# Performance work log

Measured on AMD Instinct MI355X. Metric: run time of the kernel, lower is better.

## Reference

```python
import jax, jax.numpy as jnp
import numpy as np

DIM = 1024
HEAD_DIM = 64
NUM_HEADS = DIM // HEAD_DIM
SCALE = HEAD_DIM ** -0.5
B, N, M = 2, 1024, 2048


def setup_inputs() -> dict:
    key = jax.random.key(0)
    ks = jax.random.split(key, 7)
    x = jax.random.normal(ks[0], (B, N, DIM), dtype=jnp.float32)
    context = jax.random.normal(ks[1], (B, M, DIM), dtype=jnp.float32)
    # query row has at least one valid key (avoids all -inf softmax rows).
    mask = jax.random.bernoulli(ks[2], 0.9, (B, N, M))
    mask = mask.at[:, :, 0].set(True)
    # Linear params (torch nn.Linear convention: y = x @ W.T + b)
    sq = (1.0 / DIM) ** 0.5
    Wq = jax.random.uniform(ks[3], (DIM, DIM), minval=-sq, maxval=sq, dtype=jnp.float32)
    Wkv = jax.random.uniform(ks[4], (2 * DIM, DIM), minval=-sq, maxval=sq, dtype=jnp.float32)
    b_kv = jax.random.uniform(ks[5], (2 * DIM,), minval=-sq, maxval=sq, dtype=jnp.float32)
    Wo = jax.random.uniform(ks[6], (DIM, DIM), minval=-sq, maxval=sq, dtype=jnp.float32)
    return {"x": x, "context": context, "mask": mask,
            "Wq": Wq, "Wkv": Wkv, "b_kv": b_kv, "Wo": Wo}


def reference(x, context, mask, Wq, Wkv, b_kv, Wo):
    b, n, c = x.shape
    m = context.shape[1]
    h, d = NUM_HEADS, HEAD_DIM
    # Q projection (no bias): [b, n, h, d] -> bhnd
    q = (x @ Wq.T).reshape(b, n, h, d).transpose(0, 2, 1, 3)
    # KV projection (with bias): [b, m, 2, h, d]
    kv = (context @ Wkv.T + b_kv).reshape(b, m, 2, h, d)
    k = kv[:, :, 0].transpose(0, 2, 1, 3)  # bhmd
    v = kv[:, :, 1].transpose(0, 2, 1, 3)  # bhmd
    # scores: bhnm, scale applied after matmul as in the original
    attn = jnp.einsum('bhnd,bhmd->bhnm', q, k) * SCALE
    attn = jnp.where(mask[:, None, :, :], attn, -jnp.inf)
    attn = jax.nn.softmax(attn, axis=-1)
    out = jnp.einsum('bhnm,bhmd->bhnd', attn, v)
    out = out.transpose(0, 2, 1, 3).reshape(b, n, h * d)
    return out @ Wo.T
```

## Files before the change

kernel.cpp:

```cpp
#include <hip/hip_runtime.h>


typedef __attribute__((ext_vector_type(8))) short short8;
typedef __attribute__((ext_vector_type(4))) short short4v;
typedef __attribute__((ext_vector_type(4))) float f32x4;
typedef __attribute__((ext_vector_type(4))) int int4v;

#define SCL2E 0.18033688011112042592f

__device__ __forceinline__ float bf2f(short s) {
  unsigned u = ((unsigned)(unsigned short)s) << 16;
  return __uint_as_float(u);
}
__device__ __forceinline__ short f2bf(float f) {
  unsigned u = __float_as_uint(f);
  u += 0x7fffu + ((u >> 16) & 1u);
  return (short)(u >> 16);
}
__device__ __forceinline__ int cvt_pk_bf16(float a, float b) {
  int r;
  asm("v_cvt_pk_bf16_f32 %0, %1, %2" : "=v"(r) : "v"(a), "v"(b));
  return r;
}
__device__ __forceinline__ void gld_lds16(const void* gp, void* lp) {
  __builtin_amdgcn_global_load_lds(
      (const __attribute__((address_space(1))) unsigned int*)gp,
      (__attribute__((address_space(3))) unsigned int*)lp, 16, 0, 0);
}
__device__ __forceinline__ void pipesync() {
  asm volatile("s_waitcnt vmcnt(0) lgkmcnt(0)" ::: "memory");
  __builtin_amdgcn_sched_barrier(0);
  __builtin_amdgcn_s_barrier();
  __builtin_amdgcn_sched_barrier(0);
}
__device__ __forceinline__ short4v cvt4(float4 v) {
  short4v o;
  o[0] = f2bf(v.x); o[1] = f2bf(v.y); o[2] = f2bf(v.z); o[3] = f2bf(v.w);
  return o;
}
__device__ __forceinline__ size_t off128(int row, int k) {
  return ((size_t)(((row >> 7) * 32 + (k >> 5)) * 8 + ((row >> 4) & 7)) << 9) +
         (((((k >> 3) & 3) * 16 + (row & 15)) << 3) + (k & 7));
}
__device__ __forceinline__ size_t off64(int row, int k) {
  return ((size_t)(((row >> 6) * 32 + (k >> 5)) * 4 + ((row >> 4) & 3)) << 9) +
         (((((k >> 3) & 3) * 16 + (row & 15)) << 3) + (k & 7));
}

__global__ __launch_bounds__(256) void prep(
    const unsigned char* __restrict__ mask, unsigned long long* __restrict__ pm,
    const float* __restrict__ Wq, const float* __restrict__ Wkv,
    const float* __restrict__ Wo, const float* __restrict__ x,
    const float* __restrict__ ctx, short* __restrict__ wqb,
    short* __restrict__ wkvb, short* __restrict__ wob,
    short* __restrict__ xb, short* __restrict__ ctxb) {
  const int row = blockIdx.x;
  const int wave = threadIdx.x >> 6, lane = threadIdx.x & 63;
  const unsigned char p8 = mask[lane * 4 + 1];
  const int p32 = ((const int*)mask)[lane * 2 + 1];
  const int shift =
      (__ballot(p8 != 0) != 0ull) ? 0 : ((__ballot(p32 != 0) != 0ull) ? 2 : 3);
  const size_t mbase = ((size_t)row * 2048) << shift;
#pragma unroll
  for (int j = 0; j < 8; j++) {
    const int c = wave * 512 + j * 64 + lane;
    const unsigned long long bits = __ballot(mask[mbase + ((size_t)c << shift)] != 0);
    if (lane == 0) pm[(size_t)row * 32 + wave * 8 + j] = bits;
  }
  const int gid = blockIdx.x * 256 + threadIdx.x;
  {
    const int e = gid * 4, r = e >> 10, k = e & 1023;
    *(short4v*)(xb + off128(r, k)) = cvt4(((const float4*)x)[gid]);
  }
  {
    int e = gid * 4, r = e >> 10, k = e & 1023;
    *(short4v*)(ctxb + off128(r, k)) = cvt4(((const float4*)ctx)[gid]);
    e = (gid + 524288) * 4; r = e >> 10; k = e & 1023;
    *(short4v*)(ctxb + off128(r, k)) = cvt4(((const float4*)ctx)[gid + 524288]);
  }
  {
    const int e = gid * 4, r = e >> 10, k = e & 1023;
    *(short4v*)(wkvb + off128(r, k)) = cvt4(((const float4*)Wkv)[gid]);
  }
  if (gid < 262144) {
    const int e = gid * 4, r = e >> 10, k = e & 1023;
    *(short4v*)(wqb + off128(r, k)) = cvt4(((const float4*)Wq)[gid]);
    *(short4v*)(wob + off64(r, k)) = cvt4(((const float4*)Wo)[gid]);
  }
}

__global__ __launch_bounds__(256, 2)
void qkv_gemm(const short* __restrict__ xb, const short* __restrict__ ctxb,
              const short* __restrict__ wqb, const short* __restrict__ wkvb,
              const float* __restrict__ bias, short* __restrict__ qws,
              short* __restrict__ kws, short* __restrict__ vtws) {
  __shared__ __align__(16) short ldsA[2][4096];
  __shared__ __align__(16) short ldsB[2][4096];
  const int tid = threadIdx.x;
  const int wave = tid >> 6, lane = tid & 63;
  const int l15 = lane & 15, lg = lane >> 4;
  const int bx = blockIdx.x;
  const bool isKV = bx < 512;
  const int rt = isKV ? (bx >> 4) : ((bx - 512) >> 3);
  const int ct = isKV ? (bx & 15) : ((bx - 512) & 7);
  const short* Amat = isKV ? ctxb : xb;
  const short* Bw = isKV ? wkvb : wqb;
  const int wr = wave >> 1, wc = wave & 1;

  f32x4 acc[4][4];
#pragma unroll
  for (int i = 0; i < 4; i++)
#pragma unroll
    for (int j = 0; j < 4; j++) acc[i][j] = (f32x4){0.f, 0.f, 0.f, 0.f};

  const short* ga0 = Amat + (size_t)rt * 131072 + wave * 512 + lane * 8;
  const short* ga1 = ga0 + 2048;
  const short* gb0 = Bw + (size_t)ct * 131072 + wave * 512 + lane * 8;
  const short* gb1 = gb0 + 2048;

  auto stage = [&](int kk, short* dA, short* dB) {
    const size_t koff = (size_t)kk * 4096;
    gld_lds16(ga0 + koff, dA + wave * 512);
    gld_lds16(ga1 + koff, dA + (wave + 4) * 512);
    gld_lds16(gb0 + koff, dB + wave * 512);
    gld_lds16(gb1 + koff, dB + (wave + 4) * 512);
  };
  auto compute = [&](const short* sA, const short* sB) {
    short8 af[4], bfr[4];
#pragma unroll
    for (int t = 0; t < 4; t++)
      af[t] = *(const short8*)&sA[((wr * 4 + t) * 64 + lane) * 8];
#pragma unroll
    for (int t = 0; t < 4; t++)
      bfr[t] = *(const short8*)&sB[((wc * 4 + t) * 64 + lane) * 8];
#pragma unroll
    for (int i = 0; i < 4; i++)
#pragma unroll
      for (int j = 0; j < 4; j++)
        acc[i][j] =
            __builtin_amdgcn_mfma_f32_16x16x32_bf16(af[i], bfr[j], acc[i][j], 0, 0, 0);
  };

  stage(0, ldsA[0], ldsB[0]);
  pipesync();
  for (int kk = 0; kk < 32; kk += 2) {
    if (kk + 1 < 32) stage(kk + 1, ldsA[1], ldsB[1]);
    compute(ldsA[0], ldsB[0]);
    pipesync();
    if (kk + 2 < 32) stage(kk + 2, ldsA[0], ldsB[0]);
    compute(ldsA[1], ldsB[1]);
    pipesync();
  }

#pragma unroll
  for (int i = 0; i < 4; i++)
#pragma unroll
    for (int j = 0; j < 4; j++)
#pragma unroll
      for (int r = 0; r < 4; r++) {
        const int gr = rt * 128 + wr * 64 + i * 16 + lg * 4 + r;
        const int gc = ct * 128 + wc * 64 + j * 16 + l15;
        float v = acc[i][j][r];
        if (isKV) {
          v += bias[gc];
          const int b = gr >> 11, m = gr & 2047;
          const int kv = gc >> 10, hh = (gc >> 6) & 15, d = gc & 63;
          if (kv == 0)
            kws[((((size_t)b * 16 + hh) * 2048 + m) << 6) + d] = f2bf(v);
          else {
            const int mp = (m & ~31) | (((m >> 2) & 3) << 3) |
                           (((m >> 4) & 1) << 2) | (m & 3);
            vtws[(((size_t)b * 16 + hh) * 64 + d) * 2048 + mp] = f2bf(v);
          }
        } else {
          const int b = gr >> 10, n = gr & 1023, hh = gc >> 6, d = gc & 63;
          qws[((((size_t)b * 16 + hh) * 1024 + n) << 6) + d] = f2bf(v * SCL2E);
        }
      }
}

__global__ __launch_bounds__(512, 4)
void attn_split(const short* __restrict__ Qg, const short* __restrict__ Kg,
                const short* __restrict__ Vtg,
                const unsigned int* __restrict__ pm,
                float* __restrict__ opart, float* __restrict__ lpart) {
  __shared__ __align__(16) short ldsK[2][8192];
  __shared__ __align__(16) short ldsV[2][8192];
  const int tid = threadIdx.x;
  const int w = tid >> 6, lane = tid & 63;
  const int l15 = lane & 15, lg = lane >> 4;
  const int bx = blockIdx.x;
  const int bhid = bx & 31, qt = (bx >> 5) & 7, half = bx >> 8;
  const int b = bhid >> 4, h = bhid & 15;
  const int n0 = qt * 128, m_base = half * 1024;
  const size_t bh = (size_t)b * 16 + h;
  const short* Qb = Qg + (bh * 1024 + n0) * 64;
  const short* Kb = Kg + (bh << 17);
  const short* Vb = Vtg + (bh << 17);
  const unsigned int* pmw =
      pm + ((size_t)(b * 1024 + n0 + w * 16 + l15) << 6) + (m_base >> 5);

  auto stageKV = [&](int c, short* dK, short* dV) {
    const int m0 = m_base + c * 128;
#pragma unroll
    for (int ii = 0; ii < 2; ii++) {
      const int f = w * 2 + ii;
      const int t = f >> 1, ks = f & 1;
      gld_lds16(Kb + (size_t)(m0 + t * 16 + l15) * 64 + ks * 32 + lg * 8,
                dK + f * 512);
      const int vt = f >> 2, vk = f & 3;
      gld_lds16(Vb + (size_t)(vt * 16 + l15) * 2048 + (m0 + vk * 32 + lg * 8),
                dV + f * 512);
    }
  };

#pragma unroll
  for (int ii = 0; ii < 2; ii++)
    gld_lds16(Qb + (size_t)(w * 16 + l15) * 64 + ii * 32 + lg * 8,
              &ldsK[0][(w * 2 + ii) * 512]);
  stageKV(0, ldsK[1], ldsV[1]);
  pipesync();
  short8 qf[2];
#pragma unroll
  for (int ks = 0; ks < 2; ks++)
    qf[ks] = *(const short8*)&ldsK[0][((w * 2 + ks) * 64 + lane) * 8];
  asm volatile("s_waitcnt lgkmcnt(0)" ::: "memory");
  __builtin_amdgcn_sched_barrier(0);
  __builtin_amdgcn_s_barrier();
  __builtin_amdgcn_sched_barrier(0);

  short8 onesf;
#pragma unroll
  for (int i = 0; i < 8; i++) onesf[i] = (short)0x3F80;

  f32x4 o[4], lacc;
#pragma unroll
  for (int ct = 0; ct < 4; ct++) o[ct] = (f32x4){0.f, 0.f, 0.f, 0.f};
  lacc = (f32x4){0.f, 0.f, 0.f, 0.f};
  const int sb = lg * 4;

  auto computeC = [&](int c, const short* sK, const short* sV) {
    const uint4 mk = *(const uint4*)(pmw + c * 4);
    int4v pw4[4];
#pragma unroll
    for (int h2 = 0; h2 < 2; h2++) {
      f32x4 s[4];
#pragma unroll
      for (int t2 = 0; t2 < 4; t2++) s[t2] = (f32x4){0.f, 0.f, 0.f, 0.f};
#pragma unroll
      for (int t2 = 0; t2 < 4; t2++) {
        const int t = h2 * 4 + t2;
#pragma unroll
        for (int ks = 0; ks < 2; ks++) {
          const short8 kf = *(const short8*)&sK[((t * 2 + ks) * 64 + lane) * 8];
          s[t2] = __builtin_amdgcn_mfma_f32_16x16x32_bf16(kf, qf[ks], s[t2], 0, 0, 0);
        }
      }
#pragma unroll
      for (int t2 = 0; t2 < 4; t2++) {
        const int t = h2 * 4 + t2;
        const unsigned int mw = ((t >> 1) == 0) ? mk.x
                              : ((t >> 1) == 1) ? mk.y
                              : ((t >> 1) == 2) ? mk.z : mk.w;
        float p[4];
#pragma unroll
        for (int r = 0; r < 4; r++) {
          const bool att = (mw >> (((t & 1) << 4) + sb + r)) & 1;
          p[r] = exp2f(att ? s[t2][r] : -1e30f);
        }
        pw4[t >> 1][(t & 1) * 2] = cvt_pk_bf16(p[0], p[1]);
        pw4[t >> 1][(t & 1) * 2 + 1] = cvt_pk_bf16(p[2], p[3]);
      }
    }
#pragma unroll
    for (int ks2 = 0; ks2 < 4; ks2++) {
      const short8 pf = __builtin_bit_cast(short8, pw4[ks2]);
#pragma unroll
      for (int ct = 0; ct < 4; ct++) {
        const short8 vf = *(const short8*)&sV[((ct * 4 + ks2) * 64 + lane) * 8];
        o[ct] = __builtin_amdgcn_mfma_f32_16x16x32_bf16(pf, vf, o[ct], 0, 0, 0);
      }
      lacc = __builtin_amdgcn_mfma_f32_16x16x32_bf16(pf, onesf, lacc, 0, 0, 0);
    }
  };

  for (int c = 0; c < 8; c += 2) {
    if (c + 1 < 8) stageKV(c + 1, ldsK[0], ldsV[0]);
    computeC(c, ldsK[1], ldsV[1]);
    pipesync();
    if (c + 2 < 8) stageKV(c + 2, ldsK[1], ldsV[1]);
    computeC(c + 1, ldsK[0], ldsV[0]);
    pipesync();
  }

#pragma unroll
  for (int ct = 0; ct < 4; ct++)
#pragma unroll
    for (int r = 0; r < 4; r++) {
      const int n = n0 + w * 16 + lg * 4 + r;
      opart[((size_t)half << 21) + (((size_t)b * 1024 + n) << 10) + h * 64 +
            ct * 16 + l15] = o[ct][r];
    }
  if (l15 == 0) {
#pragma unroll
    for (int r = 0; r < 4; r++) {
      const int n = n0 + w * 16 + lg * 4 + r;
      lpart[((size_t)half << 15) + bh * 1024 + n] = lacc[r];
    }
  }
}

__global__ __launch_bounds__(256) void combine(
    const float* __restrict__ opart, const float* __restrict__ lpart,
    short* __restrict__ aoT) {
  const int gid = blockIdx.x * 256 + threadIdx.x;
  const size_t base = (size_t)gid * 4;
  const int row = (int)(base >> 10), col = (int)(base & 1023);
  const int b = row >> 10, n = row & 1023, h = col >> 6;
  const float4 o1 = *(const float4*)(opart + base);
  const float4 o2 = *(const float4*)(opart + (1u << 21) + base);
  const float l1 = lpart[(size_t)(b * 16 + h) * 1024 + n];
  const float l2 = lpart[(1u << 15) + (size_t)(b * 16 + h) * 1024 + n];
  const float inv = 1.f / fmaxf(l1 + l2, 1e-30f);
  short4v o;
  o[0] = f2bf((o1.x + o2.x) * inv); o[1] = f2bf((o1.y + o2.y) * inv);
  o[2] = f2bf((o1.z + o2.z) * inv); o[3] = f2bf((o1.w + o2.w) * inv);
  *(short4v*)(aoT + off64(row, col)) = o;
}

__global__ __launch_bounds__(256, 2)
void o_gemm(const short* __restrict__ aoT, const short* __restrict__ wobT,
            float* __restrict__ Of) {
  __shared__ __align__(16) short ldsA[2][2048];
  __shared__ __align__(16) short ldsB[2][2048];
  const int tid = threadIdx.x;
  const int w = tid >> 6, lane = tid & 63;
  const int l15 = lane & 15, lg = lane >> 4;
  const int bx = blockIdx.x;
  const int rt = bx >> 4, ct = bx & 15;

  f32x4 acc[4];
#pragma unroll
  for (int j = 0; j < 4; j++) acc[j] = (f32x4){0.f, 0.f, 0.f, 0.f};

  const short* ga = aoT + (size_t)rt * 65536 + w * 512 + lane * 8;
  const short* gb = wobT + (size_t)ct * 65536 + w * 512 + lane * 8;

  auto stage = [&](int kk, short* dA, short* dB) {
    const size_t koff = (size_t)kk * 2048;
    gld_lds16(ga + koff, dA + w * 512);
    gld_lds16(gb + koff, dB + w * 512);
  };
  auto compute = [&](const short* sA, const short* sB) {
    const short8 af = *(const short8*)&sA[(w * 64 + lane) * 8];
#pragma unroll
    for (int j = 0; j < 4; j++) {
      const short8 bf = *(const short8*)&sB[(j * 64 + lane) * 8];
      acc[j] = __builtin_amdgcn_mfma_f32_16x16x32_bf16(af, bf, acc[j], 0, 0, 0);
    }
  };

  stage(0, ldsA[0], ldsB[0]);
  pipesync();
  for (int kk = 0; kk < 32; kk += 2) {
    if (kk + 1 < 32) stage(kk + 1, ldsA[1], ldsB[1]);
    compute(ldsA[0], ldsB[0]);
    pipesync();
    if (kk + 2 < 32) stage(kk + 2, ldsA[0], ldsB[0]);
    compute(ldsA[1], ldsB[1]);
    pipesync();
  }

#pragma unroll
  for (int j = 0; j < 4; j++)
#pragma unroll
    for (int r = 0; r < 4; r++) {
      const int gr = rt * 64 + w * 16 + lg * 4 + r;
      const int gc = ct * 64 + j * 16 + l15;
      Of[(size_t)gr * 1024 + gc] = acc[j][r];
    }
}

extern "C" void kernel_launch(void* const* d_in, const int* in_sizes, int n_in,
                              void* d_out, int out_size, void* d_ws, size_t ws_size,
                              hipStream_t stream) {
  const float* x   = (const float*)d_in[0];
  const float* ctx = (const float*)d_in[1];
  const unsigned char* mask = (const unsigned char*)d_in[2];
  const float* Wq  = (const float*)d_in[3];
  const float* Wkv = (const float*)d_in[4];
  const float* bkv = (const float*)d_in[5];
  const float* Wo  = (const float*)d_in[6];
  float* out = (float*)d_out;

  char* wsb = (char*)d_ws;
  short* qws  = (short*)(wsb);
  short* kws  = (short*)(wsb + (4u << 20));
  short* vtws = (short*)(wsb + (12u << 20));
  short* wqb  = (short*)(wsb + (20u << 20));
  short* wkvb = (short*)(wsb + (22u << 20));
  short* wob  = (short*)(wsb + (26u << 20));
  unsigned long long* pmws = (unsigned long long*)(wsb + (28u << 20));
  float* opart = (float*)(wsb + (29u << 20));
  float* lpart = (float*)(wsb + (45u << 20));
  short* xb   = (short*)(wsb + (29u << 20));
  short* ctxb = (short*)(wsb + (33u << 20));
  short* ao = (short*)(wsb + (20u << 20));

  prep<<<2048, 256, 0, stream>>>(mask, pmws, Wq, Wkv, Wo, x, ctx,
                                 wqb, wkvb, wob, xb, ctxb);
  qkv_gemm<<<640, 256, 0, stream>>>(xb, ctxb, wqb, wkvb, bkv, qws, kws, vtws);
  attn_split<<<512, 512, 0, stream>>>(qws, kws, vtws, (const unsigned int*)pmws,
                                      opart, lpart);
  combine<<<2048, 256, 0, stream>>>(opart, lpart, ao);
  o_gemm<<<512, 256, 0, stream>>>(ao, wob, out);
}
```

Baseline: 235.6 us.

## Triple-buffer LDS pipelines and swizzle block order in projection GEMMs

Converts the QKV and output projection GEMMs from a double-buffered stage/compute loop to a three-buffer ring. Each step uses a partial vmcnt wait with a single barrier, so two tiles stay in flight while one is computed. It also remaps block indices so consecutive blocks spread across groups, aiming for better cache/XCD locality. QKV launch bounds go up to 3 blocks per CU, which adds LDS use and register pressure. The wait-count logic depends on the exact number of global-load-to-LDS ops per stage, and the compute reads have no lgkm wait before the next overwrite barrier, which is a correctness risk.

```diff
diff --git a/kernel.cpp b/kernel.cpp
--- a/kernel.cpp
+++ b/kernel.cpp
@@ -27,6 +27,13 @@
       (const __attribute__((address_space(1))) unsigned int*)gp,
       (__attribute__((address_space(3))) unsigned int*)lp, 16, 0, 0);
 }
+__device__ __forceinline__ void sbar() {
+  __builtin_amdgcn_sched_barrier(0);
+  __builtin_amdgcn_s_barrier();
+  __builtin_amdgcn_sched_barrier(0);
+}
+#define WAITVM(N) asm volatile("s_waitcnt vmcnt(" #N ")" ::: "memory")
+
 __device__ __forceinline__ void pipesync() {
   asm volatile("s_waitcnt vmcnt(0) lgkmcnt(0)" ::: "memory");
   __builtin_amdgcn_sched_barrier(0);
@@ -89,17 +96,18 @@
   }
 }
 
-__global__ __launch_bounds__(256, 2)
+__global__ __launch_bounds__(256, 3)
 void qkv_gemm(const short* __restrict__ xb, const short* __restrict__ ctxb,
               const short* __restrict__ wqb, const short* __restrict__ wkvb,
               const float* __restrict__ bias, short* __restrict__ qws,
               short* __restrict__ kws, short* __restrict__ vtws) {
-  __shared__ __align__(16) short ldsA[2][4096];
-  __shared__ __align__(16) short ldsB[2][4096];
+  __shared__ __align__(16) short ldsA[3][4096];
+  __shared__ __align__(16) short ldsB[3][4096];
   const int tid = threadIdx.x;
   const int wave = tid >> 6, lane = tid & 63;
   const int l15 = lane & 15, lg = lane >> 4;
-  const int bx = blockIdx.x;
+  const int bx0 = blockIdx.x;
+  const int bx = (bx0 & 7) * 80 + (bx0 >> 3);
   const bool isKV = bx < 512;
   const int rt = isKV ? (bx >> 4) : ((bx - 512) >> 3);
   const int ct = isKV ? (bx & 15) : ((bx - 512) & 7);
@@ -118,14 +126,18 @@
   const short* gb0 = Bw + (size_t)ct * 131072 + wave * 512 + lane * 8;
   const short* gb1 = gb0 + 2048;
 
-  auto stage = [&](int kk, short* dA, short* dB) {
+  auto stage = [&](int kk, int buf) {
     const size_t koff = (size_t)kk * 4096;
+    short* dA = &ldsA[buf][0];
+    short* dB = &ldsB[buf][0];
     gld_lds16(ga0 + koff, dA + wave * 512);
     gld_lds16(ga1 + koff, dA + (wave + 4) * 512);
     gld_lds16(gb0 + koff, dB + wave * 512);
     gld_lds16(gb1 + koff, dB + (wave + 4) * 512);
   };
-  auto compute = [&](const short* sA, const short* sB) {
+  auto compute = [&](int buf) {
+    const short* sA = &ldsA[buf][0];
+    const short* sB = &ldsB[buf][0];
     short8 af[4], bfr[4];
 #pragma unroll
     for (int t = 0; t < 4; t++)
@@ -141,16 +153,24 @@
             __builtin_amdgcn_mfma_f32_16x16x32_bf16(af[i], bfr[j], acc[i][j], 0, 0, 0);
   };
 
-  stage(0, ldsA[0], ldsB[0]);
-  pipesync();
-  for (int kk = 0; kk < 32; kk += 2) {
-    if (kk + 1 < 32) stage(kk + 1, ldsA[1], ldsB[1]);
-    compute(ldsA[0], ldsB[0]);
-    pipesync();
-    if (kk + 2 < 32) stage(kk + 2, ldsA[0], ldsB[0]);
-    compute(ldsA[1], ldsB[1]);
-    pipesync();
-  }
+  stage(0, 0);
+  stage(1, 1);
+  int cur = 0, nxt = 2;
+  for (int i = 0; i < 30; ++i) {
+    WAITVM(4);
+    sbar();
+    stage(i + 2, nxt);
+    compute(cur);
+    cur = (cur == 2) ? 0 : cur + 1;
+    nxt = (nxt == 2) ? 0 : nxt + 1;
+  }
+  WAITVM(4);
+  sbar();
+  compute(cur);
+  cur = (cur == 2) ? 0 : cur + 1;
+  WAITVM(0);
+  sbar();
+  compute(cur);
 
 #pragma unroll
   for (int i = 0; i < 4; i++)
@@ -331,12 +351,13 @@
 __global__ __launch_bounds__(256, 2)
 void o_gemm(const short* __restrict__ aoT, const short* __restrict__ wobT,
             float* __restrict__ Of) {
-  __shared__ __align__(16) short ldsA[2][2048];
-  __shared__ __align__(16) short ldsB[2][2048];
+  __shared__ __align__(16) short ldsA[3][2048];
+  __shared__ __align__(16) short ldsB[3][2048];
   const int tid = threadIdx.x;
   const int w = tid >> 6, lane = tid & 63;
   const int l15 = lane & 15, lg = lane >> 4;
-  const int bx = blockIdx.x;
+  const int bx0 = blockIdx.x;
+  const int bx = (bx0 & 7) * 64 + (bx0 >> 3);
   const int rt = bx >> 4, ct = bx & 15;
 
   f32x4 acc[4];
@@ -346,12 +367,14 @@
   const short* ga = aoT + (size_t)rt * 65536 + w * 512 + lane * 8;
   const short* gb = wobT + (size_t)ct * 65536 + w * 512 + lane * 8;
 
-  auto stage = [&](int kk, short* dA, short* dB) {
+  auto stage = [&](int kk, int buf) {
     const size_t koff = (size_t)kk * 2048;
-    gld_lds16(ga + koff, dA + w * 512);
-    gld_lds16(gb + koff, dB + w * 512);
-  };
-  auto compute = [&](const short* sA, const short* sB) {
+    gld_lds16(ga + koff, &ldsA[buf][0] + w * 512);
+    gld_lds16(gb + koff, &ldsB[buf][0] + w * 512);
+  };
+  auto compute = [&](int buf) {
+    const short* sA = &ldsA[buf][0];
+    const short* sB = &ldsB[buf][0];
     const short8 af = *(const short8*)&sA[(w * 64 + lane) * 8];
 #pragma unroll
     for (int j = 0; j < 4; j++) {
@@ -360,16 +383,24 @@
     }
   };
 
-  stage(0, ldsA[0], ldsB[0]);
-  pipesync();
-  for (int kk = 0; kk < 32; kk += 2) {
-    if (kk + 1 < 32) stage(kk + 1, ldsA[1], ldsB[1]);
-    compute(ldsA[0], ldsB[0]);
-    pipesync();
-    if (kk + 2 < 32) stage(kk + 2, ldsA[0], ldsB[0]);
-    compute(ldsA[1], ldsB[1]);
-    pipesync();
-  }
+  stage(0, 0);
+  stage(1, 1);
+  int cur = 0, nxt = 2;
+  for (int i = 0; i < 30; ++i) {
+    WAITVM(2);
+    sbar();
+    stage(i + 2, nxt);
+    compute(cur);
+    cur = (cur == 2) ? 0 : cur + 1;
+    nxt = (nxt == 2) ? 0 : nxt + 1;
+  }
+  WAITVM(2);
+  sbar();
+  compute(cur);
+  cur = (cur == 2) ? 0 : cur + 1;
+  WAITVM(0);
+  sbar();
+  compute(cur);
 
 #pragma unroll
   for (int j = 0; j < 4; j++)
```

Measured after the change: 229.9 us. 1.02x faster.
